# Kernel optimization log

Hardware: AMD Instinct MI355X
Metric: run time of the kernel (lower is better)

The kernel has to match this reference:

```python
import jax, jax.numpy as jnp
import numpy as np

N, E = 50000, 800000
IN, MAP, H, O = 256, 64, 4, 64
LEAKY_SLOPE = 0.2


def setup_inputs() -> dict:
    key = jax.random.key(0)
    ks = jax.random.split(key, 12)
    x = jax.random.normal(ks[0], (N, IN), dtype=jnp.float32)
    src = jax.random.randint(ks[1], (E,), 0, N, dtype=jnp.int32)
    dst = jax.random.randint(ks[2], (E,), 0, N, dtype=jnp.int32)
    s = 1.0 / np.sqrt(IN)
    W_gat = jax.random.normal(ks[3], (IN, H * O), dtype=jnp.float32) * s
    attn_l = jax.random.normal(ks[4], (H, O), dtype=jnp.float32) * 0.1
    attn_r = jax.random.normal(ks[5], (H, O), dtype=jnp.float32) * 0.1
    gate_m_W = jax.random.normal(ks[6], (IN, MAP), dtype=jnp.float32) * s
    gate_m_b = jnp.zeros((MAP,), dtype=jnp.float32)
    gate_fn_W = jax.random.normal(ks[7], (2 * IN + MAP, H), dtype=jnp.float32) * (1.0 / np.sqrt(2 * IN + MAP))
    gate_fn_b = jnp.zeros((H,), dtype=jnp.float32)
    merge_W = jax.random.normal(ks[8], (IN + O, O), dtype=jnp.float32) * (1.0 / np.sqrt(IN + O))
    merge_b = jnp.zeros((O,), dtype=jnp.float32)
    return {"x": x, "src": src, "dst": dst, "W_gat": W_gat, "attn_l": attn_l,
            "attn_r": attn_r, "gate_m_W": gate_m_W, "gate_m_b": gate_m_b,
            "gate_fn_W": gate_fn_W, "gate_fn_b": gate_fn_b,
            "merge_W": merge_W, "merge_b": merge_b}


def _forward(x, src, dst, W_gat, attn_l, attn_r, gate_m_W, gate_m_b,
             gate_fn_W, gate_fn_b, merge_W, merge_b):
    n = x.shape[0]
    # --- gate branch: gspmm mean of x, gspmm max of linear_z over in-neighbors ---
    deg = jax.ops.segment_sum(jnp.ones_like(dst, dtype=x.dtype), dst, num_segments=n)
    mean_z = jax.ops.segment_sum(x[src], dst, num_segments=n) / jnp.maximum(deg, 1.0)[:, None]
    z = x @ gate_m_W + gate_m_b  # [N, MAP]
    max_z = jax.ops.segment_max(z[src], dst, num_segments=n)
    max_z = jnp.where(deg[:, None] > 0, max_z, 0.0)  # empty neighborhoods -> 0
    nft = jnp.concatenate([x, max_z, mean_z], axis=1)  # [N, 2*IN+MAP]
    gate = jax.nn.sigmoid(nft @ gate_fn_W + gate_fn_b)  # [N, H]
    # --- GATConv ---
    feat = (x @ W_gat).reshape(n, H, O)  # [N, H, O]
    el = jnp.einsum('nho,ho->nh', feat, attn_l)
    er = jnp.einsum('nho,ho->nh', feat, attn_r)
    e = jax.nn.leaky_relu(el[src] + er[dst], negative_slope=LEAKY_SLOPE)  # [E, H]
    m = jax.ops.segment_max(e, dst, num_segments=n)  # [N, H]
    m = jnp.where(jnp.isfinite(m), m, 0.0)
    ex = jnp.exp(e - m[dst])  # [E, H]
    s = jax.ops.segment_sum(ex, dst, num_segments=n)  # [N, H]
    alpha = ex / jnp.maximum(s[dst], 1e-16)  # [E, H]
    attn_out = jax.ops.segment_sum(feat[src] * alpha[:, :, None], dst, num_segments=n)  # [N, H, O]
    # --- gated merge ---
    gated = (gate[:, :, None] * attn_out).mean(axis=1)  # [N, O]
    merge = jnp.concatenate([x, gated], axis=1) @ merge_W + merge_b  # [N, O]
    return merge


def reference(x, src, dst, W_gat, attn_l, attn_r, gate_m_W, gate_m_b,
              gate_fn_W, gate_fn_b, merge_W, merge_b):
    return _forward(x, src, dst, W_gat, attn_l, attn_r, gate_m_W, gate_m_b,
                    gate_fn_W, gate_fn_b, merge_W, merge_b)
```

## Files before the change

### kernel.cpp

```cpp
#include <hip/hip_runtime.h>
#include <math.h>

#define NN 50000
#define NE 800000
#define LEAKY 0.2f
#define NT 26
#define CAP 96
#define NBT (8 * NT * 64)
#define NRB 3125
#define PACK_BLKS 6250
#define BT_BLKS 54
#define INIT_BLKS 196

typedef short bf16x8 __attribute__((ext_vector_type(8)));
typedef float f32x4 __attribute__((ext_vector_type(4)));
typedef float f32x2 __attribute__((ext_vector_type(2)));

__device__ __forceinline__ unsigned short f2bf(float f) {
  unsigned u = __float_as_uint(f);
  u += 0x7fffu + ((u >> 16) & 1u);
  return (unsigned short)(u >> 16);
}
__device__ __forceinline__ float leaky(float v) { return v > 0.0f ? v : LEAKY * v; }
__device__ __forceinline__ float rlf(float v, int l) {
  return __uint_as_float(__builtin_amdgcn_readlane(__float_as_uint(v), l));
}
__device__ __forceinline__ int rli(int v, int l) {
  return __builtin_amdgcn_readlane(v, l);
}

#if defined(__has_builtin)
#if __has_builtin(__builtin_amdgcn_cvt_pk_f32_fp8) && \
    __has_builtin(__builtin_amdgcn_cvt_pk_fp8_f32) && \
    __has_builtin(__builtin_amdgcn_cvt_f32_fp8)
#define FP8_HW 1
#endif
#endif

#ifdef FP8_HW
__device__ __forceinline__ unsigned char f2fp8(float v) {
  return (unsigned char)(__builtin_amdgcn_cvt_pk_fp8_f32(v, v, 0u, false) & 0xFF);
}
__device__ __forceinline__ f32x2 fp8x2_lo(unsigned int v) {
  return __builtin_amdgcn_cvt_pk_f32_fp8(v, false);
}
__device__ __forceinline__ f32x2 fp8x2_hi(unsigned int v) {
  return __builtin_amdgcn_cvt_pk_f32_fp8(v, true);
}
__device__ __forceinline__ float fp8one(unsigned int v) {
  return __builtin_amdgcn_cvt_f32_fp8(v, 0);
}
#else
__device__ __forceinline__ unsigned char f2fp8(float f) {
  unsigned u = __float_as_uint(f);
  unsigned s = (u >> 31) << 7;
  unsigned a = u & 0x7FFFFFFFu;
  if (a >= 0x43E00000u) return (unsigned char)(s | 0x7E);
  if (a < 0x3C800000u) {
    float m = __uint_as_float(a) * 512.0f;
    int q = (int)(m + 0.5f); if (q > 7) q = 7;
    return (unsigned char)(s | q);
  }
  a += 0x7FFFFu + ((a >> 20) & 1);
  unsigned e = ((a >> 23) & 0xFF) - 120;
  if (e > 15) return (unsigned char)(s | 0x7E);
  return (unsigned char)(s | (e << 3) | ((a >> 20) & 7));
}
__device__ __forceinline__ float fp8dec1(unsigned b) {
  unsigned s = (b & 0x80u) << 24;
  unsigned em = b & 0x7Fu;
  unsigned e4 = em >> 3, m3 = em & 7;
  float v = e4 ? __uint_as_float(((e4 + 120) << 23) | (m3 << 20))
               : (float)m3 * 0.001953125f;
  return __uint_as_float(__float_as_uint(v) ^ s);
}
__device__ __forceinline__ f32x2 fp8x2_lo(unsigned int v) {
  f32x2 r; r[0] = fp8dec1(v & 0xFF); r[1] = fp8dec1((v >> 8) & 0xFF); return r;
}
__device__ __forceinline__ f32x2 fp8x2_hi(unsigned int v) {
  f32x2 r; r[0] = fp8dec1((v >> 16) & 0xFF); r[1] = fp8dec1((v >> 24) & 0xFF); return r;
}
__device__ __forceinline__ float fp8one(unsigned int v) { return fp8dec1(v & 0xFF); }
#endif

__device__ __forceinline__ float panel_w(int col, int k,
    const float* W_gat, const float* gate_m_W, const float* merge_W,
    const float* gate_fn_W) {
  if (col < 256)      return W_gat[k * 256 + (col & 3) * 64 + (col >> 2)];
  else if (col < 320) return gate_m_W[k * 64 + (col - 256)];
  else if (col < 384) return merge_W[k * 64 + (col - 320)];
  else if (col < 388) return gate_fn_W[k * 4 + (col - 384)];
  else if (col < 392) return gate_fn_W[(320 + k) * 4 + (col - 388)];
  return 0.0f;
}

__global__ __launch_bounds__(256) void k_prep(
    const float* __restrict__ x, const float* __restrict__ W_gat,
    const float* __restrict__ gate_m_W, const float* __restrict__ merge_W,
    const float* __restrict__ gate_fn_W,
    unsigned short* __restrict__ xf, unsigned short* __restrict__ Btf,
    unsigned short* __restrict__ mWf,
    int* __restrict__ cursor, unsigned char* __restrict__ zq,
    float* __restrict__ epay, unsigned char* __restrict__ featq) {
  int b = blockIdx.x, tid = threadIdx.x;
  if (b < PACK_BLKS) {
    int gid = b * 256 + tid;
    int rowblk = gid >> 9;
    int rem = gid & 511;
    int kq = rem >> 6, lane = rem & 63;
    int m = lane & 15, kg = lane >> 4;
    const float* p = x + (size_t)(rowblk * 16 + m) * 256 + kq * 32 + kg * 8;
    float4 fa = *(const float4*)p;
    float4 fb = *(const float4*)(p + 4);
    ushort4 o0, o1;
    o0.x = f2bf(fa.x); o0.y = f2bf(fa.y); o0.z = f2bf(fa.z); o0.w = f2bf(fa.w);
    o1.x = f2bf(fb.x); o1.y = f2bf(fb.y); o1.z = f2bf(fb.z); o1.w = f2bf(fb.w);
    ushort4* dst = (ushort4*)(xf + (size_t)gid * 8);
    dst[0] = o0; dst[1] = o1;
  } else if (b < PACK_BLKS + BT_BLKS) {
    int idx = (b - PACK_BLKS) * 256 + tid;
    if (idx < NBT) {
      int kq = idx / (NT * 64);
      int rem = idx - kq * (NT * 64);
      int t = rem >> 6, lane = rem & 63;
      int col = t * 16 + (lane & 15);
      int k = kq * 32 + (lane >> 4) * 8;
      unsigned short* o = Btf + (size_t)idx * 8;
#pragma unroll
      for (int i = 0; i < 8; ++i)
        o[i] = f2bf(panel_w(col, k + i, W_gat, gate_m_W, merge_W, gate_fn_W));
    } else if (idx < NBT + 512) {
      int idx2 = idx - NBT;
      int kq = idx2 >> 8;
      int rem = idx2 & 255;
      int t = rem >> 6, lane = rem & 63;
      int col = t * 16 + (lane & 15);
      int k = kq * 32 + ((lane >> 4) & 3) * 8;
      unsigned short* o = mWf + (size_t)idx2 * 8;
#pragma unroll
      for (int i = 0; i < 8; ++i)
        o[i] = f2bf(merge_W[(size_t)(256 + k + i) * 64 + col]);
    }
  } else {
    int i = (b - PACK_BLKS - BT_BLKS) * 256 + tid;
    if (i < NN) cursor[i] = 0;
    if (b == PACK_BLKS + BT_BLKS) {
      if (tid < 64) zq[(size_t)NN * 64 + tid] = 0xFE;
      if (tid < 8) epay[(size_t)NN * 8 + tid] = 0.0f;
      featq[(size_t)NN * 256 + tid] = 0;
    }
  }
}

__global__ void k_scatter(const int* __restrict__ src, const int* __restrict__ dst,
                          int* __restrict__ cursor, unsigned short* __restrict__ csr_src) {
  int e = blockIdx.x * 256 + threadIdx.x;
  if (e < NE) {
    int n = dst[e];
    int pos = atomicAdd(&cursor[n], 1);
    if (pos < CAP) csr_src[n * CAP + pos] = (unsigned short)src[e];
  }
}

__global__ __launch_bounds__(256, 2) void k_gemm_mfma(
    const unsigned short* __restrict__ xf, const unsigned short* __restrict__ Btf,
    const float* __restrict__ gate_m_b,
    const float* __restrict__ attn_l, const float* __restrict__ attn_r,
    unsigned char* __restrict__ featq, unsigned char* __restrict__ zq,
    float* __restrict__ xm, float* __restrict__ gx, float* __restrict__ epay,
    float* __restrict__ erv) {
  __shared__ float els[64][4][2];
  __shared__ float ers[64][4][2];
  int lane = threadIdx.x & 63;
  int wave = threadIdx.x >> 6;
  int rowHalf = wave >> 1, colHalf = wave & 1;
  int rowB = blockIdx.x * 64;
  int row0 = rowB + rowHalf * 32;
  int t0 = colHalf * 13;
  int m = lane & 15, kg = lane >> 4;
  f32x4 zero = {0.f, 0.f, 0.f, 0.f};
  f32x4 acc[2][13];
#pragma unroll
  for (int g = 0; g < 2; ++g)
#pragma unroll
    for (int t = 0; t < 13; ++t) acc[g][t] = zero;

  const unsigned short* aB0 = xf + ((size_t)((blockIdx.x * 4 + rowHalf * 2) * 8) * 64 + lane) * 8;
  const unsigned short* aB1 = aB0 + (size_t)8 * 64 * 8;
  const unsigned short* bB = Btf + (size_t)(t0 * 64 + lane) * 8;

  bf16x8 aC0, aC1, aN0, aN1, bC[13], bN[13];
  aC0 = *(const bf16x8*)(aB0);
  aC1 = *(const bf16x8*)(aB1);
#pragma unroll
  for (int t = 0; t < 13; ++t)
    bC[t] = *(const bf16x8*)(bB + (size_t)t * 512);
#pragma unroll 1
  for (int kq = 0; kq < 8; kq += 2) {
    aN0 = *(const bf16x8*)(aB0 + (size_t)(kq + 1) * 512);
    aN1 = *(const bf16x8*)(aB1 + (size_t)(kq + 1) * 512);
#pragma unroll
    for (int t = 0; t < 13; ++t)
      bN[t] = *(const bf16x8*)(bB + ((size_t)(kq + 1) * NT + t) * 512);
#pragma unroll
    for (int t = 0; t < 13; ++t)
      acc[0][t] = __builtin_amdgcn_mfma_f32_16x16x32_bf16(aC0, bC[t], acc[0][t], 0, 0, 0);
#pragma unroll
    for (int t = 0; t < 13; ++t)
      acc[1][t] = __builtin_amdgcn_mfma_f32_16x16x32_bf16(aC1, bC[t], acc[1][t], 0, 0, 0);
    int kq2 = kq + 2 < 8 ? kq + 2 : 7;
    aC0 = *(const bf16x8*)(aB0 + (size_t)kq2 * 512);
    aC1 = *(const bf16x8*)(aB1 + (size_t)kq2 * 512);
#pragma unroll
    for (int t = 0; t < 13; ++t)
      bC[t] = *(const bf16x8*)(bB + ((size_t)kq2 * NT + t) * 512);
#pragma unroll
    for (int t = 0; t < 13; ++t)
      acc[0][t] = __builtin_amdgcn_mfma_f32_16x16x32_bf16(aN0, bN[t], acc[0][t], 0, 0, 0);
#pragma unroll
    for (int t = 0; t < 13; ++t)
      acc[1][t] = __builtin_amdgcn_mfma_f32_16x16x32_bf16(aN1, bN[t], acc[1][t], 0, 0, 0);
  }

  int h = m & 3, od = m >> 2;
  float elp[2][4] = {{0,0,0,0},{0,0,0,0}}, erp[2][4] = {{0,0,0,0},{0,0,0,0}};
#pragma unroll
  for (int t = 0; t < 13; ++t) {
    if ((t0 + t) * 16 < 256) {
      int o = (t0 + t) * 4 + od;
      float al = attn_l[h * 64 + o];
      float ar = attn_r[h * 64 + o];
#pragma unroll
      for (int g = 0; g < 2; ++g)
#pragma unroll
        for (int r = 0; r < 4; ++r) {
          elp[g][r] += acc[g][t][r] * al;
          erp[g][r] += acc[g][t][r] * ar;
        }
    }
  }
#pragma unroll
  for (int g = 0; g < 2; ++g)
#pragma unroll
    for (int r = 0; r < 4; ++r) {
      elp[g][r] += __shfl_xor(elp[g][r], 4, 64); elp[g][r] += __shfl_xor(elp[g][r], 8, 64);
      erp[g][r] += __shfl_xor(erp[g][r], 4, 64); erp[g][r] += __shfl_xor(erp[g][r], 8, 64);
    }
  if (m < 4) {
#pragma unroll
    for (int g = 0; g < 2; ++g)
#pragma unroll
      for (int r = 0; r < 4; ++r) {
        els[rowHalf * 32 + g * 16 + kg * 4 + r][m][colHalf] = elp[g][r];
        ers[rowHalf * 32 + g * 16 + kg * 4 + r][m][colHalf] = erp[g][r];
      }
  }

#pragma unroll
  for (int g = 0; g < 2; ++g) {
    if (colHalf == 0) {
#pragma unroll
      for (int r = 0; r < 4; ++r) {
        int row = row0 + g * 16 + kg * 4 + r;
        if (row >= NN) continue;
#pragma unroll
        for (int t = 0; t < 13; ++t)
          featq[(size_t)row * 256 + t * 16 + m] = f2fp8(acc[g][t][r]);
      }
    } else {
#pragma unroll
      for (int r = 0; r < 4; ++r) {
        int row = row0 + g * 16 + kg * 4 + r;
        if (row >= NN) continue;
#pragma unroll
        for (int t = 0; t < 3; ++t)
          featq[(size_t)row * 256 + 208 + t * 16 + m] = f2fp8(acc[g][t][r]);
#pragma unroll
        for (int t = 3; t < 7; ++t) {
          int cc = (t - 3) * 16 + m;
          zq[(size_t)row * 64 + cc] = f2fp8(acc[g][t][r] + gate_m_b[cc]);
        }
#pragma unroll
        for (int t = 7; t < 11; ++t)
          xm[(size_t)row * 64 + (t - 7) * 16 + m] = acc[g][t][r];
        if (m < 4) gx[(size_t)row * 4 + m] = acc[g][11][r];
        else if (m < 8) epay[(size_t)row * 8 + (m - 4) * 2 + 1] = acc[g][11][r];
      }
    }
  }
  __syncthreads();
  int tid = threadIdx.x;
  {
    int rr = tid >> 2, h2 = tid & 3;
    int row = rowB + rr;
    if (row < NN) {
      epay[(size_t)row * 8 + h2 * 2] = els[rr][h2][0] + els[rr][h2][1];
      erv[(size_t)row * 4 + h2] = ers[rr][h2][0] + ers[rr][h2][1];
    }
  }
}

__global__ __launch_bounds__(256) void k_node(
    const unsigned char* __restrict__ zq, const unsigned char* __restrict__ featq,
    const float* __restrict__ epay, const float* __restrict__ er,
    const float* __restrict__ gx,
    const int* __restrict__ cursor, const unsigned short* __restrict__ csr_src,
    const float* __restrict__ gate_fn_W, const float* __restrict__ gate_fn_b,
    const unsigned short* __restrict__ mWf, const float* __restrict__ xm,
    const float* __restrict__ merge_b, float* __restrict__ out) {
  __shared__ float WzT[4][64];
  __shared__ float pbuf[4][16][4];
  __shared__ unsigned short gLDS[16][72];
  int tid = threadIdx.x;
  {
    int c = tid >> 2, h = tid & 3;
    WzT[h][c] = gate_fn_W[(256 + c) * 4 + h];
  }
  __syncthreads();

  int lane = tid & 63, wave = tid >> 6;
  int hh = lane >> 4, le = lane & 15;
  int nodeBase = blockIdx.x * 16 + wave * 4;
#pragma unroll 1
  for (int i = 0; i < 4; ++i) {
    int node = nodeBase + i;
    int deg = cursor[node]; if (deg > CAP) deg = CAP;
    float gated = 0.0f;
    if (deg > 0) {
      int rs = node * CAP, re = rs + deg;
      float er_h = er[(size_t)node * 4 + hh];
      f32x2 A01 = {0.f, 0.f}, A23 = {0.f, 0.f};
      float psum = 0, usum = 0;
      float mz = -INFINITY;
      int jj = rs + le;
      int s_l = (jj < re) ? (int)csr_src[jj] : NN;
#pragma unroll 1
      for (int j0 = rs; j0 < re; j0 += 16) {
        int jn = j0 + 16 + le;
        int s_nx = (jn < re) ? (int)csr_src[jn] : NN;
        bool valid = (j0 + le) < re;
        float2 eu = *(const float2*)(epay + ((size_t)(unsigned)s_l << 3) + hh * 2);
        float p = valid ? __expf(leaky(eu.x + er_h)) : 0.0f;
        psum += p;
        usum += eu.y;
        pbuf[wave][le][hh] = p;
        unsigned int fvr[16];
        unsigned int zvr[16];
#pragma unroll
        for (int e2 = 0; e2 < 16; ++e2) {
          int s = rli(s_l, e2);
          fvr[e2] = *(const unsigned int*)(featq + ((size_t)(unsigned)s << 8) + lane * 4);
        }
#pragma unroll
        for (int e2 = 0; e2 < 16; ++e2) {
          int s = rli(s_l, e2);
          zvr[e2] = zq[((size_t)(unsigned)s << 6) + lane];
        }
#pragma unroll
        for (int e2 = 0; e2 < 16; ++e2) {
          float4 pv = *(const float4*)pbuf[wave][e2];
          f32x2 p01 = {pv.x, pv.y};
          f32x2 p23 = {pv.z, pv.w};
          A01 += p01 * fp8x2_lo(fvr[e2]);
          A23 += p23 * fp8x2_hi(fvr[e2]);
          mz = fmaxf(mz, fp8one(zvr[e2]));
        }
        s_l = s_nx;
      }
#pragma unroll
      for (int off = 1; off < 16; off <<= 1) {
        psum += __shfl_xor(psum, off, 64);
        usum += __shfl_xor(usum, off, 64);
      }
      float s0 = rlf(psum, 0),  s1 = rlf(psum, 16);
      float s2 = rlf(psum, 32), s3 = rlf(psum, 48);
      float su0 = rlf(usum, 0),  su1 = rlf(usum, 16);
      float su2 = rlf(usum, 32), su3 = rlf(usum, 48);

      float g[4];
#pragma unroll
      for (int h = 0; h < 4; ++h) {
        float t = mz * WzT[h][lane];
#pragma unroll
        for (int off = 32; off; off >>= 1) t += __shfl_xor(t, off, 64);
        g[h] = t;
      }
      float inv_deg = 1.0f / (float)deg;
      float4 gx4 = *(const float4*)(gx + (size_t)node * 4);
      float g0 = 1.0f / (1.0f + __expf(-(g[0] + gx4.x + su0 * inv_deg + gate_fn_b[0])));
      float g1 = 1.0f / (1.0f + __expf(-(g[1] + gx4.y + su1 * inv_deg + gate_fn_b[1])));
      float g2 = 1.0f / (1.0f + __expf(-(g[2] + gx4.z + su2 * inv_deg + gate_fn_b[2])));
      float g3 = 1.0f / (1.0f + __expf(-(g[3] + gx4.w + su3 * inv_deg + gate_fn_b[3])));
      gated = 0.25f * (g0 * A01[0] / s0 + g1 * A01[1] / s1 +
                       g2 * A23[0] / s2 + g3 * A23[1] / s3);
    }
    gLDS[wave * 4 + i][lane] = f2bf(gated);
  }
  __syncthreads();

  int m = lane & 15, kg = lane >> 4;
  f32x4 acc = {0.f, 0.f, 0.f, 0.f};
#pragma unroll
  for (int kq = 0; kq < 2; ++kq) {
    bf16x8 a = *(const bf16x8*)(&gLDS[m][kq * 32 + kg * 8]);
    bf16x8 b = *(const bf16x8*)(mWf + (((size_t)kq * 4 + wave) * 64 + lane) * 8);
    acc = __builtin_amdgcn_mfma_f32_16x16x32_bf16(a, b, acc, 0, 0, 0);
  }
  int c = wave * 16 + m;
  float mb = merge_b[c];
#pragma unroll
  for (int r = 0; r < 4; ++r) {
    int row = blockIdx.x * 16 + kg * 4 + r;
    out[(size_t)row * 64 + c] = acc[r] + xm[(size_t)row * 64 + c] + mb;
  }
}

extern "C" void kernel_launch(void* const* d_in, const int* in_sizes, int n_in,
                              void* d_out, int out_size, void* d_ws, size_t ws_size,
                              hipStream_t stream) {
  const float* x         = (const float*)d_in[0];
  const int*   src       = (const int*)d_in[1];
  const int*   dst       = (const int*)d_in[2];
  const float* W_gat     = (const float*)d_in[3];
  const float* attn_l    = (const float*)d_in[4];
  const float* attn_r    = (const float*)d_in[5];
  const float* gate_m_W  = (const float*)d_in[6];
  const float* gate_m_b  = (const float*)d_in[7];
  const float* gate_fn_W = (const float*)d_in[8];
  const float* gate_fn_b = (const float*)d_in[9];
  const float* merge_W   = (const float*)d_in[10];
  const float* merge_b   = (const float*)d_in[11];
  float* out = (float*)d_out;

  char* ws = (char*)d_ws;
  size_t off = 0;
  auto alloc = [&](size_t bytes) -> void* {
    off = (off + 255) & ~(size_t)255;
    void* p = ws + off;
    off += bytes;
    return p;
  };
  int* cursor    = (int*)alloc((size_t)NN * 4);
  unsigned short* csr_src = (unsigned short*)alloc((size_t)NN * CAP * 2);
  float* epay = (float*)alloc((size_t)(NN + 1) * 8 * 4);
  float* er   = (float*)alloc((size_t)NN * 4 * 4);
  float* gx   = (float*)alloc((size_t)NN * 4 * 4);
  float* xm   = (float*)alloc((size_t)NN * 64 * 4);
  unsigned char* zq    = (unsigned char*)alloc((size_t)(NN + 1) * 64);
  unsigned char* featq = (unsigned char*)alloc((size_t)(NN + 1) * 256);
  unsigned short* xf     = (unsigned short*)alloc((size_t)(NRB + 4) * 512 * 8 * 2);
  unsigned short* Btf    = (unsigned short*)alloc((size_t)NBT * 8 * 2);
  unsigned short* mWf    = (unsigned short*)alloc((size_t)512 * 8 * 2);

  k_prep<<<PACK_BLKS + BT_BLKS + INIT_BLKS, 256, 0, stream>>>(
      x, W_gat, gate_m_W, merge_W, gate_fn_W, xf, Btf, mWf, cursor, zq, epay, featq);
  k_scatter<<<(NE + 255) / 256, 256, 0, stream>>>(src, dst, cursor, csr_src);
  k_gemm_mfma<<<(NN + 63) / 64, 256, 0, stream>>>(xf, Btf, gate_m_b, attn_l, attn_r,
                                                  featq, zq, xm, gx, epay, er);
  k_node<<<NN / 16, 256, 0, stream>>>(zq, featq, epay, er, gx, cursor, csr_src,
                                      gate_fn_W, gate_fn_b, mWf, xm, merge_b, out);
}
```

Baseline: 245.5 us.

## Fuse x bf16 conversion into GEMM A-loads and drop the pre-pack pass

Removes the separate pass that converted x to a packed bf16 layout. The GEMM now reads fp32 x directly and converts to bf16 in registers with v_cvt_pk_bf16_f32, which avoids writing and re-reading a bf16 copy of x. The cursor array is now zeroed with hipMemsetAsync, and the node kernel is split into two launches with a row base offset. The trade-off is that the GEMM's A loads become strided fp32 row reads at twice the bytes, and the split adds a kernel launch.

Result: slower. 273.1 us (+11.2%).

```diff
diff --git a/kernel.cpp b/kernel.cpp
--- a/kernel.cpp
+++ b/kernel.cpp
@@ -7,10 +7,7 @@
 #define NT 26
 #define CAP 96
 #define NBT (8 * NT * 64)
-#define NRB 3125
-#define PACK_BLKS 6250
 #define BT_BLKS 54
-#define INIT_BLKS 196
 
 typedef short bf16x8 __attribute__((ext_vector_type(8)));
 typedef float f32x4 __attribute__((ext_vector_type(4)));
@@ -27,6 +24,19 @@
 }
 __device__ __forceinline__ int rli(int v, int l) {
   return __builtin_amdgcn_readlane(v, l);
+}
+
+__device__ __forceinline__ bf16x8 ld_a_bf16(const float* p) {
+  float4 fa = *(const float4*)p;
+  float4 fb = *(const float4*)(p + 4);
+  unsigned r0, r1, r2, r3;
+  asm("v_cvt_pk_bf16_f32 %0, %1, %2" : "=v"(r0) : "v"(fa.x), "v"(fa.y));
+  asm("v_cvt_pk_bf16_f32 %0, %1, %2" : "=v"(r1) : "v"(fa.z), "v"(fa.w));
+  asm("v_cvt_pk_bf16_f32 %0, %1, %2" : "=v"(r2) : "v"(fb.x), "v"(fb.y));
+  asm("v_cvt_pk_bf16_f32 %0, %1, %2" : "=v"(r3) : "v"(fb.z), "v"(fb.w));
+  union { uint4 u; bf16x8 v; } c;
+  c.u = make_uint4(r0, r1, r2, r3);
+  return c.v;
 }
 
 #if defined(__has_builtin)
@@ -95,60 +105,38 @@
 }
 
 __global__ __launch_bounds__(256) void k_prep(
-    const float* __restrict__ x, const float* __restrict__ W_gat,
-    const float* __restrict__ gate_m_W, const float* __restrict__ merge_W,
-    const float* __restrict__ gate_fn_W,
-    unsigned short* __restrict__ xf, unsigned short* __restrict__ Btf,
-    unsigned short* __restrict__ mWf,
-    int* __restrict__ cursor, unsigned char* __restrict__ zq,
-    float* __restrict__ epay, unsigned char* __restrict__ featq) {
+    const float* __restrict__ W_gat, const float* __restrict__ gate_m_W,
+    const float* __restrict__ merge_W, const float* __restrict__ gate_fn_W,
+    unsigned short* __restrict__ Btf, unsigned short* __restrict__ mWf,
+    unsigned char* __restrict__ zq, float* __restrict__ epay,
+    unsigned char* __restrict__ featq) {
   int b = blockIdx.x, tid = threadIdx.x;
-  if (b < PACK_BLKS) {
-    int gid = b * 256 + tid;
-    int rowblk = gid >> 9;
-    int rem = gid & 511;
-    int kq = rem >> 6, lane = rem & 63;
-    int m = lane & 15, kg = lane >> 4;
-    const float* p = x + (size_t)(rowblk * 16 + m) * 256 + kq * 32 + kg * 8;
-    float4 fa = *(const float4*)p;
-    float4 fb = *(const float4*)(p + 4);
-    ushort4 o0, o1;
-    o0.x = f2bf(fa.x); o0.y = f2bf(fa.y); o0.z = f2bf(fa.z); o0.w = f2bf(fa.w);
-    o1.x = f2bf(fb.x); o1.y = f2bf(fb.y); o1.z = f2bf(fb.z); o1.w = f2bf(fb.w);
-    ushort4* dst = (ushort4*)(xf + (size_t)gid * 8);
-    dst[0] = o0; dst[1] = o1;
-  } else if (b < PACK_BLKS + BT_BLKS) {
-    int idx = (b - PACK_BLKS) * 256 + tid;
-    if (idx < NBT) {
-      int kq = idx / (NT * 64);
-      int rem = idx - kq * (NT * 64);
-      int t = rem >> 6, lane = rem & 63;
-      int col = t * 16 + (lane & 15);
-      int k = kq * 32 + (lane >> 4) * 8;
-      unsigned short* o = Btf + (size_t)idx * 8;
-#pragma unroll
-      for (int i = 0; i < 8; ++i)
-        o[i] = f2bf(panel_w(col, k + i, W_gat, gate_m_W, merge_W, gate_fn_W));
-    } else if (idx < NBT + 512) {
-      int idx2 = idx - NBT;
-      int kq = idx2 >> 8;
-      int rem = idx2 & 255;
-      int t = rem >> 6, lane = rem & 63;
-      int col = t * 16 + (lane & 15);
-      int k = kq * 32 + ((lane >> 4) & 3) * 8;
-      unsigned short* o = mWf + (size_t)idx2 * 8;
-#pragma unroll
-      for (int i = 0; i < 8; ++i)
-        o[i] = f2bf(merge_W[(size_t)(256 + k + i) * 64 + col]);
-    }
-  } else {
-    int i = (b - PACK_BLKS - BT_BLKS) * 256 + tid;
-    if (i < NN) cursor[i] = 0;
-    if (b == PACK_BLKS + BT_BLKS) {
-      if (tid < 64) zq[(size_t)NN * 64 + tid] = 0xFE;
-      if (tid < 8) epay[(size_t)NN * 8 + tid] = 0.0f;
-      featq[(size_t)NN * 256 + tid] = 0;
-    }
+  int idx = b * 256 + tid;
+  if (idx < NBT) {
+    int kq = idx / (NT * 64);
+    int rem = idx - kq * (NT * 64);
+    int t = rem >> 6, lane = rem & 63;
+    int col = t * 16 + (lane & 15);
+    int k = kq * 32 + (lane >> 4) * 8;
+    unsigned short* o = Btf + (size_t)idx * 8;
+#pragma unroll
+    for (int i = 0; i < 8; ++i)
+      o[i] = f2bf(panel_w(col, k + i, W_gat, gate_m_W, merge_W, gate_fn_W));
+  } else if (idx < NBT + 512) {
+    int idx2 = idx - NBT;
+    int kq = idx2 >> 8;
+    int rem = idx2 & 255;
+    int t = rem >> 6, lane = rem & 63;
+    int col = t * 16 + (lane & 15);
+    int k = kq * 32 + ((lane >> 4) & 3) * 8;
+    unsigned short* o = mWf + (size_t)idx2 * 8;
+#pragma unroll
+    for (int i = 0; i < 8; ++i)
+      o[i] = f2bf(merge_W[(size_t)(256 + k + i) * 64 + col]);
+  } else if (b == BT_BLKS) {
+    if (tid < 64) zq[(size_t)NN * 64 + tid] = 0xFE;
+    if (tid < 8) epay[(size_t)NN * 8 + tid] = 0.0f;
+    featq[(size_t)NN * 256 + tid] = 0;
   }
 }
 
@@ -163,7 +151,7 @@
 }
 
 __global__ __launch_bounds__(256, 2) void k_gemm_mfma(
-    const unsigned short* __restrict__ xf, const unsigned short* __restrict__ Btf,
+    const float* __restrict__ x, const unsigned short* __restrict__ Btf,
     const float* __restrict__ gate_m_b,
     const float* __restrict__ attn_l, const float* __restrict__ attn_r,
     unsigned char* __restrict__ featq, unsigned char* __restrict__ zq,
@@ -185,20 +173,24 @@
 #pragma unroll
     for (int t = 0; t < 13; ++t) acc[g][t] = zero;
 
-  const unsigned short* aB0 = xf + ((size_t)((blockIdx.x * 4 + rowHalf * 2) * 8) * 64 + lane) * 8;
-  const unsigned short* aB1 = aB0 + (size_t)8 * 64 * 8;
+  int r0i = row0 + m;
+  int r1i = r0i + 16;
+  if (r0i >= NN) r0i = NN - 1;
+  if (r1i >= NN) r1i = NN - 1;
+  const float* aP0 = x + (size_t)r0i * 256 + kg * 8;
+  const float* aP1 = x + (size_t)r1i * 256 + kg * 8;
   const unsigned short* bB = Btf + (size_t)(t0 * 64 + lane) * 8;
 
   bf16x8 aC0, aC1, aN0, aN1, bC[13], bN[13];
-  aC0 = *(const bf16x8*)(aB0);
-  aC1 = *(const bf16x8*)(aB1);
+  aC0 = ld_a_bf16(aP0);
+  aC1 = ld_a_bf16(aP1);
 #pragma unroll
   for (int t = 0; t < 13; ++t)
     bC[t] = *(const bf16x8*)(bB + (size_t)t * 512);
 #pragma unroll 1
   for (int kq = 0; kq < 8; kq += 2) {
-    aN0 = *(const bf16x8*)(aB0 + (size_t)(kq + 1) * 512);
-    aN1 = *(const bf16x8*)(aB1 + (size_t)(kq + 1) * 512);
+    aN0 = ld_a_bf16(aP0 + (kq + 1) * 32);
+    aN1 = ld_a_bf16(aP1 + (kq + 1) * 32);
 #pragma unroll
     for (int t = 0; t < 13; ++t)
       bN[t] = *(const bf16x8*)(bB + ((size_t)(kq + 1) * NT + t) * 512);
@@ -209,8 +201,8 @@
     for (int t = 0; t < 13; ++t)
       acc[1][t] = __builtin_amdgcn_mfma_f32_16x16x32_bf16(aC1, bC[t], acc[1][t], 0, 0, 0);
     int kq2 = kq + 2 < 8 ? kq + 2 : 7;
-    aC0 = *(const bf16x8*)(aB0 + (size_t)kq2 * 512);
-    aC1 = *(const bf16x8*)(aB1 + (size_t)kq2 * 512);
+    aC0 = ld_a_bf16(aP0 + kq2 * 32);
+    aC1 = ld_a_bf16(aP1 + kq2 * 32);
 #pragma unroll
     for (int t = 0; t < 13; ++t)
       bC[t] = *(const bf16x8*)(bB + ((size_t)kq2 * NT + t) * 512);
@@ -307,7 +299,7 @@
     const int* __restrict__ cursor, const unsigned short* __restrict__ csr_src,
     const float* __restrict__ gate_fn_W, const float* __restrict__ gate_fn_b,
     const unsigned short* __restrict__ mWf, const float* __restrict__ xm,
-    const float* __restrict__ merge_b, float* __restrict__ out) {
+    const float* __restrict__ merge_b, float* __restrict__ out, int nbase) {
   __shared__ float WzT[4][64];
   __shared__ float pbuf[4][16][4];
   __shared__ unsigned short gLDS[16][72];
@@ -320,7 +312,8 @@
 
   int lane = tid & 63, wave = tid >> 6;
   int hh = lane >> 4, le = lane & 15;
-  int nodeBase = blockIdx.x * 16 + wave * 4;
+  int rowbase = nbase + blockIdx.x * 16;
+  int nodeBase = rowbase + wave * 4;
 #pragma unroll 1
   for (int i = 0; i < 4; ++i) {
     int node = nodeBase + i;
@@ -410,7 +403,7 @@
   float mb = merge_b[c];
 #pragma unroll
   for (int r = 0; r < 4; ++r) {
-    int row = blockIdx.x * 16 + kg * 4 + r;
+    int row = rowbase + kg * 4 + r;
     out[(size_t)row * 64 + c] = acc[r] + xm[(size_t)row * 64 + c] + mb;
   }
 }
@@ -448,15 +441,20 @@
   float* xm   = (float*)alloc((size_t)NN * 64 * 4);
   unsigned char* zq    = (unsigned char*)alloc((size_t)(NN + 1) * 64);
   unsigned char* featq = (unsigned char*)alloc((size_t)(NN + 1) * 256);
-  unsigned short* xf     = (unsigned short*)alloc((size_t)(NRB + 4) * 512 * 8 * 2);
   unsigned short* Btf    = (unsigned short*)alloc((size_t)NBT * 8 * 2);
   unsigned short* mWf    = (unsigned short*)alloc((size_t)512 * 8 * 2);
 
-  k_prep<<<PACK_BLKS + BT_BLKS + INIT_BLKS, 256, 0, stream>>>(
-      x, W_gat, gate_m_W, merge_W, gate_fn_W, xf, Btf, mWf, cursor, zq, epay, featq);
+  hipMemsetAsync(cursor, 0, (size_t)NN * 4, stream);
+  k_prep<<<BT_BLKS + 1, 256, 0, stream>>>(W_gat, gate_m_W, merge_W, gate_fn_W,
+                                          Btf, mWf, zq, epay, featq);
   k_scatter<<<(NE + 255) / 256, 256, 0, stream>>>(src, dst, cursor, csr_src);
-  k_gemm_mfma<<<(NN + 63) / 64, 256, 0, stream>>>(xf, Btf, gate_m_b, attn_l, attn_r,
+  k_gemm_mfma<<<(NN + 63) / 64, 256, 0, stream>>>(x, Btf, gate_m_b, attn_l, attn_r,
                                                   featq, zq, xm, gx, epay, er);
-  k_node<<<NN / 16, 256, 0, stream>>>(zq, featq, epay, er, gx, cursor, csr_src,
-                                      gate_fn_W, gate_fn_b, mWf, xm, merge_b, out);
-}
+  const int HALF1 = 1563;
+  const int HALF2 = (NN / 16) - HALF1;
+  k_node<<<HALF1, 256, 0, stream>>>(zq, featq, epay, er, gx, cursor, csr_src,
+                                    gate_fn_W, gate_fn_b, mWf, xm, merge_b, out, 0);
+  k_node<<<HALF2, 256, 0, stream>>>(zq, featq, epay, er, gx, cursor, csr_src,
+                                    gate_fn_W, gate_fn_b, mWf, xm, merge_b, out,
+                                    HALF1 * 16);
+}
```
